# Optimization experiments

Measured on AMD Instinct MI355X. Metric: run time of the kernel, lower is better.

Reference implementation:

```python
import jax, jax.numpy as jnp
import numpy as np

EPS = 1e-12  # torch F.normalize eps

def rmsnorm(x, g, dim):
    # F.normalize(x, dim=-1) * sqrt(dim) * g  (g is a learned scalar)
    n = jnp.maximum(jnp.linalg.norm(x, axis=-1, keepdims=True), EPS)
    return x / n * (dim ** 0.5) * g

def modulate(x, scale, shift):
    # x: (B,T,D); scale/shift: (B,D)
    return x * (1.0 + scale[:, None, :]) + shift[:, None, :]

def setup_inputs() -> dict:
    key = jax.random.key(0)
    ks = jax.random.split(key, 12)
    B, T, D, H = 8, 1024, 1024, 16
    Dm = 4 * D
    s = 0.02
    inp = {
        'x': jax.random.normal(ks[0], (B, T, D), jnp.float32),
        'c': jax.random.normal(ks[1], (B, D), jnp.float32),
        'g1': jnp.ones((1,), jnp.float32),
        'g2': jnp.ones((1,), jnp.float32),
        'gq': jnp.ones((1,), jnp.float32),
        'gk': jnp.ones((1,), jnp.float32),
        'Wqkv': jax.random.normal(ks[2], (3 * D, D), jnp.float32) * s,
        'bqkv': jnp.zeros((3 * D,), jnp.float32),
        'Wproj': jax.random.normal(ks[3], (D, D), jnp.float32) * s,
        'bproj': jnp.zeros((D,), jnp.float32),
        'Wfc1': jax.random.normal(ks[4], (Dm, D), jnp.float32) * s,
        'bfc1': jnp.zeros((Dm,), jnp.float32),
        'Wfc2': jax.random.normal(ks[5], (D, Dm), jnp.float32) * s,
        'bfc2': jnp.zeros((D,), jnp.float32),
        'Wada': jax.random.normal(ks[6], (6 * D, D), jnp.float32) * s,
        'bada': jnp.zeros((6 * D,), jnp.float32),
    }
    return inp

def reference(x, c, g1, g2, gq, gk, Wqkv, bqkv, Wproj, bproj,
              Wfc1, bfc1, Wfc2, bfc2, Wada, bada):
    B, T, D = x.shape
    H = 16
    hd = D // H

    # adaLN modulation: SiLU -> Linear -> chunk 6 along last dim
    ada = jax.nn.silu(c) @ Wada.T + bada  # (B, 6D)
    shift_msa, scale_msa, gate_msa, shift_mlp, scale_mlp, gate_mlp = jnp.split(ada, 6, axis=-1)

    # --- attention branch ---
    h = modulate(rmsnorm(x, g1, D), scale_msa, shift_msa)  # (B,T,D)
    qkv = h @ Wqkv.T + bqkv  # (B,T,3D)
    qkv = qkv.reshape(B, T, 3, H, hd).transpose(2, 0, 3, 1, 4)  # (3,B,H,T,hd)
    q, k, v = qkv[0], qkv[1], qkv[2]
    q = rmsnorm(q, gq, hd) * (hd ** -0.5)
    k = rmsnorm(k, gk, hd)
    attn = jax.nn.softmax(jnp.einsum('bhqd,bhkd->bhqk', q, k), axis=-1)
    o = jnp.einsum('bhqk,bhkd->bhqd', attn, v)  # (B,H,T,hd)
    o = o.transpose(0, 2, 1, 3).reshape(B, T, D)
    o = o @ Wproj.T + bproj
    x = x + gate_msa[:, None, :] * o

    # --- MLP branch ---
    h = modulate(rmsnorm(x, g2, D), scale_mlp, shift_mlp)
    h = jax.nn.gelu(h @ Wfc1.T + bfc1, approximate=True)
    h = h @ Wfc2.T + bfc2
    x = x + gate_mlp[:, None, :] * h
    return x
```

## Files before the change

### kernel.cpp

```cpp
#include <hip/hip_runtime.h>
#include <hip/hip_bf16.h>
#include <math.h>

typedef __bf16 bf16x8 __attribute__((ext_vector_type(8)));
typedef __bf16 bf16x4 __attribute__((ext_vector_type(4)));
typedef float  f32x4  __attribute__((ext_vector_type(4)));

#define DEV static __device__ __forceinline__

DEV unsigned short f2bf(float f) {
    unsigned u = __builtin_bit_cast(unsigned, f);
    u += 0x7fffu + ((u >> 16) & 1u);
    return (unsigned short)(u >> 16);
}
DEV float bf2f(unsigned short u) {
    unsigned x = ((unsigned)u) << 16;
    return __builtin_bit_cast(float, x);
}

__global__ void k_cvt(const float* __restrict__ in, unsigned short* __restrict__ out) {
    int i = (blockIdx.x * 256 + threadIdx.x) * 4;
    float4 v = *(const float4*)(in + i);
    ushort4 o;
    o.x = f2bf(v.x); o.y = f2bf(v.y); o.z = f2bf(v.z); o.w = f2bf(v.w);
    *(ushort4*)(out + i) = o;
}

__global__ void k_ada(const float* __restrict__ c, const float* __restrict__ Wada,
                      const float* __restrict__ bada, float* __restrict__ ada) {
    __shared__ float sc[1024];
    int b = blockIdx.x;
    int tid = threadIdx.x;
    for (int k = tid; k < 1024; k += 256) {
        float x = c[b * 1024 + k];
        sc[k] = x / (1.f + __expf(-x));
    }
    __syncthreads();
    int wid = tid >> 6, lane = tid & 63;
    int n = blockIdx.y * 4 + wid;
    const float* wr = Wada + (size_t)n * 1024;
    float acc = 0.f;
    #pragma unroll
    for (int k = 0; k < 1024; k += 64) acc += sc[k + lane] * wr[k + lane];
    #pragma unroll
    for (int o = 32; o; o >>= 1) acc += __shfl_xor(acc, o);
    if (lane == 0) ada[b * 6144 + n] = acc + bada[n];
}

__global__ void k_norm_mod(const float* __restrict__ x, const float* __restrict__ ada,
                           const float* __restrict__ g, unsigned short* __restrict__ h,
                           int shift_off, int scale_off) {
    int row = blockIdx.x;
    int b = row >> 10;
    int tid = threadIdx.x;
    float4 v = *(const float4*)(x + (size_t)row * 1024 + tid * 4);
    float ss = v.x * v.x + v.y * v.y + v.z * v.z + v.w * v.w;
    #pragma unroll
    for (int o = 32; o; o >>= 1) ss += __shfl_xor(ss, o);
    __shared__ float red[4];
    int wid = tid >> 6, lane = tid & 63;
    if (lane == 0) red[wid] = ss;
    __syncthreads();
    float nrm = sqrtf(red[0] + red[1] + red[2] + red[3]);
    float f = g[0] * 32.f / fmaxf(nrm, 1e-12f);
    float4 s4 = *(const float4*)(ada + b * 6144 + scale_off + tid * 4);
    float4 h4 = *(const float4*)(ada + b * 6144 + shift_off + tid * 4);
    ushort4 o;
    o.x = f2bf(v.x * f * (1.f + s4.x) + h4.x);
    o.y = f2bf(v.y * f * (1.f + s4.y) + h4.y);
    o.z = f2bf(v.z * f * (1.f + s4.z) + h4.z);
    o.w = f2bf(v.w * f * (1.f + s4.w) + h4.w);
    *(ushort4*)(h + (size_t)row * 1024 + tid * 4) = o;
}

template <int EPI>
__global__ __launch_bounds__(256)
void k_gemm(const unsigned short* __restrict__ A, const unsigned short* __restrict__ Bw,
            const float* __restrict__ bias, int N, int K,
            float* __restrict__ outF, unsigned short* __restrict__ outH,
            const float* __restrict__ resid, const float* __restrict__ ada, int gate_off) {
    __shared__ unsigned short lA[128 * 32];
    __shared__ unsigned short lB[128 * 32];
    int tid = threadIdx.x;
    int m0 = blockIdx.x * 128, n0 = blockIdx.y * 128;
    int wid = tid >> 6, lane = tid & 63;
    int wr = (wid >> 1) * 64, wc = (wid & 1) * 64;
    f32x4 acc[4][4] = {};

    for (int kk = 0; kk < K; kk += 32) {
        #pragma unroll
        for (int r = 0; r < 2; ++r) {
            int f = r * 4096 + tid * 16;
            int row = f >> 6;
            int kb = (f & 63) >> 1;
            const unsigned short* ga = A  + (size_t)(m0 + row) * K + kk + kb;
            const unsigned short* gb = Bw + (size_t)(n0 + row) * K + kk + kb;
            unsigned short* la = lA + ((r * 4096 + wid * 1024) >> 1);
            unsigned short* lb = lB + ((r * 4096 + wid * 1024) >> 1);
            __builtin_amdgcn_global_load_lds((const __attribute__((address_space(1))) void*)ga,
                                             (__attribute__((address_space(3))) void*)la, 16, 0, 0);
            __builtin_amdgcn_global_load_lds((const __attribute__((address_space(1))) void*)gb,
                                             (__attribute__((address_space(3))) void*)lb, 16, 0, 0);
        }
        __syncthreads();
        bf16x8 af[4];
        #pragma unroll
        for (int i = 0; i < 4; ++i)
            af[i] = *(const bf16x8*)(lA + (wr + i * 16 + (lane & 15)) * 32 + (lane >> 4) * 8);
        #pragma unroll
        for (int j = 0; j < 4; ++j) {
            bf16x8 bfr = *(const bf16x8*)(lB + (wc + j * 16 + (lane & 15)) * 32 + (lane >> 4) * 8);
            #pragma unroll
            for (int i = 0; i < 4; ++i)
                acc[i][j] = __builtin_amdgcn_mfma_f32_16x16x32_bf16(af[i], bfr, acc[i][j], 0, 0, 0);
        }
        __syncthreads();
    }

    int cl = lane & 15, rb = (lane >> 4) * 4;
    #pragma unroll
    for (int i = 0; i < 4; ++i) {
        #pragma unroll
        for (int j = 0; j < 4; ++j) {
            #pragma unroll
            for (int r = 0; r < 4; ++r) {
                int row = m0 + wr + i * 16 + rb + r;
                int col = n0 + wc + j * 16 + cl;
                float v = acc[i][j][r] + bias[col];
                if (EPI == 0) {
                    outH[(size_t)row * N + col] = f2bf(v);
                } else if (EPI == 2) {
                    float t = tanhf(0.7978845608f * (v + 0.044715f * v * v * v));
                    outH[(size_t)row * N + col] = f2bf(0.5f * v * (1.f + t));
                } else {
                    int b = row >> 10;
                    float gt = ada[b * 6144 + gate_off + col];
                    outF[(size_t)row * N + col] = resid[(size_t)row * N + col] + gt * v;
                }
            }
        }
    }
}

__global__ __launch_bounds__(256)
void k_qkv_post(const unsigned short* __restrict__ qkv,
                const float* __restrict__ gq, const float* __restrict__ gk,
                unsigned short* __restrict__ Qb, unsigned short* __restrict__ Kb,
                unsigned short* __restrict__ Vtg) {
    __shared__ unsigned short vt[64 * 72];
    int bh = blockIdx.x;
    int b = bh >> 4, h = bh & 15;
    int t0 = blockIdx.y * 64;
    int tid = threadIdx.x;
    int row = tid >> 2, part = tid & 3;
    size_t rbase = ((size_t)(b * 1024 + t0 + row)) * 3072 + h * 64 + part * 16;
    size_t obase = (size_t)bh * 65536 + (size_t)(t0 + row) * 64 + part * 16;

    #pragma unroll
    for (int s = 0; s < 2; ++s) {
        uint4 u0 = *(const uint4*)(qkv + rbase + s * 1024);
        uint4 u1 = *(const uint4*)(qkv + rbase + s * 1024 + 8);
        float vals[16];
        const unsigned* pu = (const unsigned*)&u0;
        #pragma unroll
        for (int j = 0; j < 4; ++j) {
            vals[2*j]   = bf2f((unsigned short)(pu[j] & 0xffff));
            vals[2*j+1] = bf2f((unsigned short)(pu[j] >> 16));
        }
        pu = (const unsigned*)&u1;
        #pragma unroll
        for (int j = 0; j < 4; ++j) {
            vals[8+2*j]   = bf2f((unsigned short)(pu[j] & 0xffff));
            vals[8+2*j+1] = bf2f((unsigned short)(pu[j] >> 16));
        }
        float ss = 0.f;
        #pragma unroll
        for (int j = 0; j < 16; ++j) ss += vals[j] * vals[j];
        ss += __shfl_xor(ss, 1);
        ss += __shfl_xor(ss, 2);
        float nrm = fmaxf(sqrtf(ss), 1e-12f);
        float fsc = (s == 0 ? gq[0] : 8.f * gk[0]) / nrm;
        uint4 w0, w1;
        unsigned* pw = (unsigned*)&w0;
        #pragma unroll
        for (int j = 0; j < 4; ++j)
            pw[j] = (unsigned)f2bf(vals[2*j] * fsc) | ((unsigned)f2bf(vals[2*j+1] * fsc) << 16);
        pw = (unsigned*)&w1;
        #pragma unroll
        for (int j = 0; j < 4; ++j)
            pw[j] = (unsigned)f2bf(vals[8+2*j] * fsc) | ((unsigned)f2bf(vals[8+2*j+1] * fsc) << 16);
        unsigned short* dst = (s == 0 ? Qb : Kb);
        *(uint4*)(dst + obase)     = w0;
        *(uint4*)(dst + obase + 8) = w1;
    }
    {
        uint4 u0 = *(const uint4*)(qkv + rbase + 2048);
        uint4 u1 = *(const uint4*)(qkv + rbase + 2048 + 8);
        const unsigned* pu = (const unsigned*)&u0;
        #pragma unroll
        for (int j = 0; j < 4; ++j) {
            vt[(part * 16 + 2*j)     * 72 + row] = (unsigned short)(pu[j] & 0xffff);
            vt[(part * 16 + 2*j + 1) * 72 + row] = (unsigned short)(pu[j] >> 16);
        }
        pu = (const unsigned*)&u1;
        #pragma unroll
        for (int j = 0; j < 4; ++j) {
            vt[(part * 16 + 8 + 2*j)     * 72 + row] = (unsigned short)(pu[j] & 0xffff);
            vt[(part * 16 + 8 + 2*j + 1) * 72 + row] = (unsigned short)(pu[j] >> 16);
        }
    }
    __syncthreads();
    {
        int d = tid >> 2, seg = tid & 3;
        uint4 w0 = *(const uint4*)(vt + d * 72 + seg * 16);
        uint4 w1 = *(const uint4*)(vt + d * 72 + seg * 16 + 8);
        size_t vdst = (size_t)bh * 65536 + (size_t)d * 1024 + t0 + seg * 16;
        *(uint4*)(Vtg + vdst)     = w0;
        *(uint4*)(Vtg + vdst + 8) = w1;
    }
}

__global__ __launch_bounds__(256)
void k_attn_mfma(const unsigned short* __restrict__ Qb,
                 const unsigned short* __restrict__ Kb,
                 const unsigned short* __restrict__ Vtg,
                 unsigned short* __restrict__ outp) {
    __shared__ unsigned short Kt[128 * 64];
    __shared__ unsigned short Vl[64 * 136];
    int bh = blockIdx.x;
    int t0 = blockIdx.y * 64;
    int tid = threadIdx.x, wid = tid >> 6, lane = tid & 63;
    int li = lane & 15, lg = lane >> 4;
    const size_t bh64k = (size_t)bh * 65536;

    bf16x8 q0, q1;
    {
        const unsigned short* Qg = Qb + bh64k + (size_t)(t0 + wid * 16 + li) * 64 + lg * 8;
        q0 = *(const bf16x8*)Qg;
        q1 = *(const bf16x8*)(Qg + 32);
    }
    f32x4 oacc[4] = {};
    float den = 0.f;

    for (int kt = 0; kt < 8; ++kt) {
        __syncthreads();
        #pragma unroll
        for (int i = 0; i < 4; ++i) {
            int s = i * 256 + tid;
            int r = s >> 3, c16 = s & 7;
            const unsigned short* src = Kb + bh64k + (size_t)(kt * 128 + r) * 64 + ((c16 ^ (r & 7)) * 8);
            unsigned short* dst = Kt + i * 2048 + wid * 512;
            __builtin_amdgcn_global_load_lds((const __attribute__((address_space(1))) void*)src,
                                             (__attribute__((address_space(3))) void*)dst, 16, 0, 0);
        }
        #pragma unroll
        for (int i = 0; i < 4; ++i) {
            int s = i * 256 + tid;
            int d = s >> 4, k16 = s & 15;
            uint4 v = *(const uint4*)(Vtg + bh64k + (size_t)d * 1024 + kt * 128 + k16 * 8);
            *(uint4*)(Vl + d * 136 + k16 * 8) = v;
        }
        __syncthreads();

        f32x4 st[8];
        #pragma unroll
        for (int f = 0; f < 8; ++f) {
            int row = f * 16 + li;
            bf16x8 a0 = *(const bf16x8*)(Kt + row * 64 + ((lg       ^ (row & 7)) * 8));
            bf16x8 a1 = *(const bf16x8*)(Kt + row * 64 + (((4 + lg) ^ (row & 7)) * 8));
            f32x4 s = {};
            s = __builtin_amdgcn_mfma_f32_16x16x32_bf16(a0, q0, s, 0, 0, 0);
            s = __builtin_amdgcn_mfma_f32_16x16x32_bf16(a1, q1, s, 0, 0, 0);
            f32x4 e;
            e[0] = __expf(s[0]); e[1] = __expf(s[1]);
            e[2] = __expf(s[2]); e[3] = __expf(s[3]);
            den += e[0] + e[1] + e[2] + e[3];
            st[f] = e;
        }
        #pragma unroll
        for (int ks = 0; ks < 4; ++ks) {
            f32x4 e0 = st[2 * ks], e1 = st[2 * ks + 1];
            bf16x8 pa;
            pa[0] = (__bf16)e0[0]; pa[1] = (__bf16)e0[1]; pa[2] = (__bf16)e0[2]; pa[3] = (__bf16)e0[3];
            pa[4] = (__bf16)e1[0]; pa[5] = (__bf16)e1[1]; pa[6] = (__bf16)e1[2]; pa[7] = (__bf16)e1[3];
            #pragma unroll
            for (int df = 0; df < 4; ++df) {
                const unsigned short* vp = Vl + (df * 16 + li) * 136 + ks * 32 + lg * 4;
                bf16x4 v0 = *(const bf16x4*)vp;
                bf16x4 v1 = *(const bf16x4*)(vp + 16);
                bf16x8 vb = __builtin_shufflevector(v0, v1, 0, 1, 2, 3, 4, 5, 6, 7);
                oacc[df] = __builtin_amdgcn_mfma_f32_16x16x32_bf16(pa, vb, oacc[df], 0, 0, 0);
            }
        }
    }
    den += __shfl_xor(den, 16);
    den += __shfl_xor(den, 32);

    int b = bh >> 4, h = bh & 15;
    #pragma unroll
    for (int r2 = 0; r2 < 4; ++r2) {
        float dm = __shfl(den, lg * 4 + r2);
        float inv = 1.f / dm;
        int t = t0 + wid * 16 + lg * 4 + r2;
        #pragma unroll
        for (int df = 0; df < 4; ++df) {
            int col = h * 64 + df * 16 + li;
            outp[((size_t)(b * 1024 + t)) * 1024 + col] = f2bf(oacc[df][r2] * inv);
        }
    }
}

extern "C" void kernel_launch(void* const* d_in, const int* in_sizes, int n_in,
                              void* d_out, int out_size, void* d_ws, size_t ws_size,
                              hipStream_t stream) {
    const float* x     = (const float*)d_in[0];
    const float* c     = (const float*)d_in[1];
    const float* g1    = (const float*)d_in[2];
    const float* g2    = (const float*)d_in[3];
    const float* gq    = (const float*)d_in[4];
    const float* gk    = (const float*)d_in[5];
    const float* Wqkv  = (const float*)d_in[6];
    const float* bqkv  = (const float*)d_in[7];
    const float* Wproj = (const float*)d_in[8];
    const float* bproj = (const float*)d_in[9];
    const float* Wfc1  = (const float*)d_in[10];
    const float* bfc1  = (const float*)d_in[11];
    const float* Wfc2  = (const float*)d_in[12];
    const float* bfc2  = (const float*)d_in[13];
    const float* Wada  = (const float*)d_in[14];
    const float* bada  = (const float*)d_in[15];
    float* out = (float*)d_out;

    char* ws = (char*)d_ws;
    unsigned short* wqkv_bf = (unsigned short*)ws; ws += (size_t)3072 * 1024 * 2;
    unsigned short* wproj_bf= (unsigned short*)ws; ws += (size_t)1024 * 1024 * 2;
    unsigned short* wfc1_bf = (unsigned short*)ws; ws += (size_t)4096 * 1024 * 2;
    unsigned short* wfc2_bf = (unsigned short*)ws; ws += (size_t)4096 * 1024 * 2;
    float* ada = (float*)ws;                       ws += (size_t)8 * 6144 * 4;
    unsigned short* hbuf = (unsigned short*)ws;    ws += (size_t)8192 * 1024 * 2;
    unsigned short* qkvb16 = (unsigned short*)ws;  ws += (size_t)8192 * 3072 * 2;
    unsigned short* Qb  = (unsigned short*)ws;     ws += (size_t)8192 * 64 * 16 * 2;
    unsigned short* Kb  = (unsigned short*)ws;     ws += (size_t)8192 * 64 * 16 * 2;
    unsigned short* Vtg = (unsigned short*)ws;     ws += (size_t)8192 * 64 * 16 * 2;
    unsigned short* fc1out = qkvb16;

    k_cvt<<<3072 * 1024 / 1024, 256, 0, stream>>>(Wqkv,  wqkv_bf);
    k_cvt<<<1024 * 1024 / 1024, 256, 0, stream>>>(Wproj, wproj_bf);
    k_cvt<<<4096 * 1024 / 1024, 256, 0, stream>>>(Wfc1,  wfc1_bf);
    k_cvt<<<4096 * 1024 / 1024, 256, 0, stream>>>(Wfc2,  wfc2_bf);
    k_ada<<<dim3(8, 1536), 256, 0, stream>>>(c, Wada, bada, ada);
    k_norm_mod<<<8192, 256, 0, stream>>>(x, ada, g1, hbuf, 0, 1024);
    k_gemm<0><<<dim3(64, 24), 256, 0, stream>>>(hbuf, wqkv_bf, bqkv, 3072, 1024,
                                                nullptr, qkvb16, nullptr, nullptr, 0);
    k_qkv_post<<<dim3(128, 16), 256, 0, stream>>>(qkvb16, gq, gk, Qb, Kb, Vtg);
    k_attn_mfma<<<dim3(128, 16), 256, 0, stream>>>(Qb, Kb, Vtg, hbuf);
    k_gemm<1><<<dim3(64, 8), 256, 0, stream>>>(hbuf, wproj_bf, bproj, 1024, 1024,
                                               out, nullptr, x, ada, 2048);
    k_norm_mod<<<8192, 256, 0, stream>>>(out, ada, g2, hbuf, 3072, 4096);
    k_gemm<2><<<dim3(64, 32), 256, 0, stream>>>(hbuf, wfc1_bf, bfc1, 4096, 1024,
                                                nullptr, fc1out, nullptr, nullptr, 0);
    k_gemm<3><<<dim3(64, 8), 256, 0, stream>>>(fc1out, wfc2_bf, bfc2, 1024, 4096,
                                               out, nullptr, out, ada, 5120);
}
```

Measured before the change: 465.0 us.

## Replace GEMM with 256-row tiled, 4-stage pipelined, swizzled-LDS 512-thread kernel

The simple 128x128 GEMM with two syncthreads per k-step is replaced by a 256xBN tile kernel using 8 waves. It adds a 4-slot LDS ring with loads issued three steps ahead, XOR-swizzled LDS layout to avoid bank conflicts, and split A-fragment loads interleaved with MFMA under s_setprio. Block IDs are remapped across XCDs for L2 locality, and the GELU tanh uses an exp-based formula. The aim is to hide global-load latency and raise MFMA utilisation in the four GEMMs, at the cost of larger LDS use and hand-tuned vmcnt waits that are fragile.

```diff
diff --git a/kernel.cpp b/kernel.cpp
--- a/kernel.cpp
+++ b/kernel.cpp
@@ -73,69 +73,133 @@
     *(ushort4*)(h + (size_t)row * 1024 + tid * 4) = o;
 }
 
-template <int EPI>
-__global__ __launch_bounds__(256)
-void k_gemm(const unsigned short* __restrict__ A, const unsigned short* __restrict__ Bw,
-            const float* __restrict__ bias, int N, int K,
-            float* __restrict__ outF, unsigned short* __restrict__ outH,
-            const float* __restrict__ resid, const float* __restrict__ ada, int gate_off) {
-    __shared__ unsigned short lA[128 * 32];
-    __shared__ unsigned short lB[128 * 32];
+template <int EPI, int BN>
+__global__ __launch_bounds__(512, 2)
+void k_gemm2(const unsigned short* __restrict__ A, const unsigned short* __restrict__ Bw,
+             const float* __restrict__ bias, int N, int K, int gridM,
+             float* __restrict__ outF, unsigned short* __restrict__ outH,
+             const float* __restrict__ resid, const float* __restrict__ ada, int gate_off) {
+    constexpr int WN = (BN == 256) ? 4 : 2;
+    constexpr int WM = 8 / WN;
+    constexpr int WR = 256 / WM;
+    constexpr int MF = WR / 16;
+    constexpr int MF2 = MF / 2;
+    constexpr int LB = BN / 128;
+    constexpr int TL = 2 + LB;
+    __shared__ unsigned short sA[4][256 * 32];
+    __shared__ unsigned short sB[4][BN * 32];
+
     int tid = threadIdx.x;
-    int m0 = blockIdx.x * 128, n0 = blockIdx.y * 128;
     int wid = tid >> 6, lane = tid & 63;
-    int wr = (wid >> 1) * 64, wc = (wid & 1) * 64;
-    f32x4 acc[4][4] = {};
-
-    for (int kk = 0; kk < K; kk += 32) {
-        #pragma unroll
-        for (int r = 0; r < 2; ++r) {
-            int f = r * 4096 + tid * 16;
-            int row = f >> 6;
-            int kb = (f & 63) >> 1;
-            const unsigned short* ga = A  + (size_t)(m0 + row) * K + kk + kb;
-            const unsigned short* gb = Bw + (size_t)(n0 + row) * K + kk + kb;
-            unsigned short* la = lA + ((r * 4096 + wid * 1024) >> 1);
-            unsigned short* lb = lB + ((r * 4096 + wid * 1024) >> 1);
-            __builtin_amdgcn_global_load_lds((const __attribute__((address_space(1))) void*)ga,
-                                             (__attribute__((address_space(3))) void*)la, 16, 0, 0);
-            __builtin_amdgcn_global_load_lds((const __attribute__((address_space(1))) void*)gb,
-                                             (__attribute__((address_space(3))) void*)lb, 16, 0, 0);
-        }
-        __syncthreads();
-        bf16x8 af[4];
-        #pragma unroll
-        for (int i = 0; i < 4; ++i)
-            af[i] = *(const bf16x8*)(lA + (wr + i * 16 + (lane & 15)) * 32 + (lane >> 4) * 8);
-        #pragma unroll
-        for (int j = 0; j < 4; ++j) {
-            bf16x8 bfr = *(const bf16x8*)(lB + (wc + j * 16 + (lane & 15)) * 32 + (lane >> 4) * 8);
+    int li = lane & 15, lg = lane >> 4;
+
+    int nwg = gridDim.x;
+    int cpx = nwg >> 3;
+    int bid = blockIdx.x;
+    int v = (bid & 7) * cpx + (bid >> 3);
+    int mb = v % gridM, nb = v / gridM;
+    int m0 = mb * 256, n0 = nb * BN;
+
+    int wr = (wid / WN) * WR, wc = (wid % WN) * 64;
+
+    int arow = tid >> 2, ag = tid & 3;
+    int afr = (arow & 3) ^ ((arow >> 2) & 3);
+    int ags = (ag ^ afr) * 8;
+    int lfr = (li & 3) ^ ((li >> 2) & 3);
+    int aoff = li * 32 + ((lg ^ lfr) * 8);
+
+    auto stageA = [&](int t) {
+        int slot = t & 3;
+        int kk = t << 5;
+        #pragma unroll
+        for (int l = 0; l < 2; ++l) {
+            int row = arow + l * 128;
+            const unsigned short* src = A + (size_t)(m0 + row) * K + kk + ags;
+            unsigned short* dst = &sA[slot][0] + (l * 512 + wid * 64) * 8;
+            __builtin_amdgcn_global_load_lds((const __attribute__((address_space(1))) void*)src,
+                                             (__attribute__((address_space(3))) void*)dst, 16, 0, 0);
+        }
+    };
+    auto stageB = [&](int t) {
+        int slot = t & 3;
+        int kk = t << 5;
+        #pragma unroll
+        for (int l = 0; l < LB; ++l) {
+            int row = arow + l * 128;
+            const unsigned short* src = Bw + (size_t)(n0 + row) * K + kk + ags;
+            unsigned short* dst = &sB[slot][0] + (l * 512 + wid * 64) * 8;
+            __builtin_amdgcn_global_load_lds((const __attribute__((address_space(1))) void*)src,
+                                             (__attribute__((address_space(3))) void*)dst, 16, 0, 0);
+        }
+    };
+
+    int NT = K >> 5;
+    stageA(0); stageB(0); stageA(1); stageB(1); stageA(2); stageB(2);
+    asm volatile("s_waitcnt vmcnt(%0)" :: "n"(2 * TL) : "memory");
+    __builtin_amdgcn_s_barrier();
+
+    f32x4 acc[MF][4] = {};
+
+    for (int t = 0; t < NT; ++t) {
+        int slot = t & 3;
+        const unsigned short* pa = &sA[slot][0];
+        const unsigned short* pb = &sB[slot][0];
+        bf16x8 bfr[4];
+        bf16x8 af[MF2];
+        if (t + 3 < NT) stageA(t + 3);
+        #pragma unroll
+        for (int nf = 0; nf < 4; ++nf)
+            bfr[nf] = *(const bf16x8*)(pb + (wc + nf * 16) * 32 + aoff);
+        #pragma unroll
+        for (int m = 0; m < MF2; ++m)
+            af[m] = *(const bf16x8*)(pa + (wr + m * 16) * 32 + aoff);
+        __builtin_amdgcn_s_barrier();
+        __builtin_amdgcn_s_setprio(1);
+        #pragma unroll
+        for (int m = 0; m < MF2; ++m)
             #pragma unroll
-            for (int i = 0; i < 4; ++i)
-                acc[i][j] = __builtin_amdgcn_mfma_f32_16x16x32_bf16(af[i], bfr, acc[i][j], 0, 0, 0);
-        }
-        __syncthreads();
-    }
-
-    int cl = lane & 15, rb = (lane >> 4) * 4;
-    #pragma unroll
-    for (int i = 0; i < 4; ++i) {
-        #pragma unroll
-        for (int j = 0; j < 4; ++j) {
+            for (int nf = 0; nf < 4; ++nf)
+                acc[m][nf] = __builtin_amdgcn_mfma_f32_16x16x32_bf16(af[m], bfr[nf], acc[m][nf], 0, 0, 0);
+        __builtin_amdgcn_s_setprio(0);
+        if (t + 3 < NT) stageB(t + 3);
+        #pragma unroll
+        for (int m = 0; m < MF2; ++m)
+            af[m] = *(const bf16x8*)(pa + (wr + (MF2 + m) * 16) * 32 + aoff);
+        __builtin_amdgcn_s_barrier();
+        __builtin_amdgcn_s_setprio(1);
+        #pragma unroll
+        for (int m = 0; m < MF2; ++m)
+            #pragma unroll
+            for (int nf = 0; nf < 4; ++nf)
+                acc[MF2 + m][nf] = __builtin_amdgcn_mfma_f32_16x16x32_bf16(af[m], bfr[nf], acc[MF2 + m][nf], 0, 0, 0);
+        __builtin_amdgcn_s_setprio(0);
+        if (t < NT - 3)       asm volatile("s_waitcnt vmcnt(%0)" :: "n"(2 * TL) : "memory");
+        else if (t == NT - 3) asm volatile("s_waitcnt vmcnt(%0)" :: "n"(TL) : "memory");
+        else if (t == NT - 2) asm volatile("s_waitcnt vmcnt(0)" ::: "memory");
+        __builtin_amdgcn_s_barrier();
+    }
+
+    int rb4 = lg * 4;
+    #pragma unroll
+    for (int mf = 0; mf < MF; ++mf) {
+        #pragma unroll
+        for (int nf = 0; nf < 4; ++nf) {
             #pragma unroll
             for (int r = 0; r < 4; ++r) {
-                int row = m0 + wr + i * 16 + rb + r;
-                int col = n0 + wc + j * 16 + cl;
-                float v = acc[i][j][r] + bias[col];
+                int row = m0 + wr + mf * 16 + rb4 + r;
+                int col = n0 + wc + nf * 16 + li;
+                float vv = acc[mf][nf][r] + bias[col];
                 if (EPI == 0) {
-                    outH[(size_t)row * N + col] = f2bf(v);
+                    outH[(size_t)row * N + col] = f2bf(vv);
                 } else if (EPI == 2) {
-                    float t = tanhf(0.7978845608f * (v + 0.044715f * v * v * v));
-                    outH[(size_t)row * N + col] = f2bf(0.5f * v * (1.f + t));
+                    float a2 = 0.7978845608f * (vv + 0.044715f * vv * vv * vv);
+                    float e = __expf(-2.f * fabsf(a2));
+                    float th = copysignf((1.f - e) / (1.f + e), a2);
+                    outH[(size_t)row * N + col] = f2bf(0.5f * vv * (1.f + th));
                 } else {
                     int b = row >> 10;
                     float gt = ada[b * 6144 + gate_off + col];
-                    outF[(size_t)row * N + col] = resid[(size_t)row * N + col] + gt * v;
+                    outF[(size_t)row * N + col] = resid[(size_t)row * N + col] + gt * vv;
                 }
             }
         }
@@ -350,15 +414,15 @@
     k_cvt<<<4096 * 1024 / 1024, 256, 0, stream>>>(Wfc2,  wfc2_bf);
     k_ada<<<dim3(8, 1536), 256, 0, stream>>>(c, Wada, bada, ada);
     k_norm_mod<<<8192, 256, 0, stream>>>(x, ada, g1, hbuf, 0, 1024);
-    k_gemm<0><<<dim3(64, 24), 256, 0, stream>>>(hbuf, wqkv_bf, bqkv, 3072, 1024,
-                                                nullptr, qkvb16, nullptr, nullptr, 0);
+    k_gemm2<0, 256><<<384, 512, 0, stream>>>(hbuf, wqkv_bf, bqkv, 3072, 1024, 32,
+                                             nullptr, qkvb16, nullptr, nullptr, 0);
     k_qkv_post<<<dim3(128, 16), 256, 0, stream>>>(qkvb16, gq, gk, Qb, Kb, Vtg);
     k_attn_mfma<<<dim3(128, 16), 256, 0, stream>>>(Qb, Kb, Vtg, hbuf);
-    k_gemm<1><<<dim3(64, 8), 256, 0, stream>>>(hbuf, wproj_bf, bproj, 1024, 1024,
-                                               out, nullptr, x, ada, 2048);
+    k_gemm2<1, 128><<<256, 512, 0, stream>>>(hbuf, wproj_bf, bproj, 1024, 1024, 32,
+                                             out, nullptr, x, ada, 2048);
     k_norm_mod<<<8192, 256, 0, stream>>>(out, ada, g2, hbuf, 3072, 4096);
-    k_gemm<2><<<dim3(64, 32), 256, 0, stream>>>(hbuf, wfc1_bf, bfc1, 4096, 1024,
-                                                nullptr, fc1out, nullptr, nullptr, 0);
-    k_gemm<3><<<dim3(64, 8), 256, 0, stream>>>(fc1out, wfc2_bf, bfc2, 1024, 4096,
-                                               out, nullptr, out, ada, 5120);
-}
+    k_gemm2<2, 256><<<512, 512, 0, stream>>>(hbuf, wfc1_bf, bfc1, 4096, 1024, 32,
+                                             nullptr, fc1out, nullptr, nullptr, 0);
+    k_gemm2<3, 128><<<256, 512, 0, stream>>>(fc1out, wfc2_bf, bfc2, 1024, 4096, 32,
+                                             out, nullptr, out, ada, 5120);
+}
```

Measured after the change: 495.4 us. 1.07x slower.
